# Optimization experiments

Measured on AMD Instinct MI355X. Metric: run time of the kernel, lower is better.

The kernel has to match this reference:

```python
import jax, jax.numpy as jnp
import numpy as np

HIDDEN = 2048
HEAD_DIM = 128
N_HEADS = 16
N_KV_HEADS = 8
Q_DIM = N_HEADS * HEAD_DIM          # 2048
K_DIM = N_KV_HEADS * HEAD_DIM       # 1024
ROPE_THETA = 1.0e6
EPS = 1e-6
T = 4096


def setup_inputs() -> dict:
    key = jax.random.key(0)
    ks = jax.random.split(key, 4)
    x = jax.random.normal(ks[0], (T, HIDDEN), dtype=jnp.float32)
    qkv_w = jax.random.normal(ks[1], (Q_DIM + 2 * K_DIM, HIDDEN), dtype=jnp.float32) * 0.02
    o_w = jax.random.normal(ks[2], (HIDDEN, Q_DIM), dtype=jnp.float32) * 0.02
    q_norm_w = jnp.ones((HEAD_DIM,), dtype=jnp.float32)
    k_norm_w = jnp.ones((HEAD_DIM,), dtype=jnp.float32)
    positions = jnp.arange(T, dtype=jnp.int64 if jax.config.jax_enable_x64 else jnp.int32)
    return {"x": x, "qkv_w": qkv_w, "q_norm_w": q_norm_w,
            "k_norm_w": k_norm_w, "o_w": o_w, "positions": positions}


def _rms_norm(v, w):
    # v: [T, H, D]; normalize over last dim
    var = jnp.mean(v * v, axis=-1, keepdims=True)
    return v * jax.lax.rsqrt(var + EPS) * w


def _rope(v, cos, sin):
    # neox style: rotate halves. v: [T, H, D]; cos/sin: [T, 1, D/2]
    half = v.shape[-1] // 2
    v1, v2 = v[..., :half], v[..., half:]
    return jnp.concatenate([v1 * cos - v2 * sin, v2 * cos + v1 * sin], axis=-1)


def reference(x, qkv_w, q_norm_w, k_norm_w, o_w, positions):
    t = x.shape[0]
    qkv = x @ qkv_w.T                                   # [T, Q_DIM+2*K_DIM]
    q = qkv[:, :Q_DIM].reshape(t, N_HEADS, HEAD_DIM)
    k = qkv[:, Q_DIM:Q_DIM + K_DIM].reshape(t, N_KV_HEADS, HEAD_DIM)
    v = qkv[:, Q_DIM + K_DIM:].reshape(t, N_KV_HEADS, HEAD_DIM)

    q = _rms_norm(q, q_norm_w)
    k = _rms_norm(k, k_norm_w)

    half = HEAD_DIM // 2
    inv_freq = 1.0 / (ROPE_THETA ** (jnp.arange(0, half, dtype=jnp.float32) / half))
    freqs = positions.astype(jnp.float32)[:, None] * inv_freq[None, :]  # [T, half]
    cos = jnp.cos(freqs)[:, None, :]                     # [T, 1, half]
    sin = jnp.sin(freqs)[:, None, :]
    q = _rope(q, cos, sin)
    k = _rope(k, cos, sin)

    # GQA: each kv head serves N_HEADS // N_KV_HEADS query heads
    rep = N_HEADS // N_KV_HEADS
    k = jnp.repeat(k, rep, axis=1)                       # [T, N_HEADS, D]
    v = jnp.repeat(v, rep, axis=1)

    scale = 1.0 / np.sqrt(HEAD_DIM)
    scores = jnp.einsum('thd,shd->hts', q, k) * scale    # [H, T, T]
    causal = positions[:, None] >= positions[None, :]    # [T, T]
    scores = jnp.where(causal[None, :, :], scores, jnp.float32(-1e9))
    attn = jax.nn.softmax(scores, axis=-1)
    o = jnp.einsum('hts,shd->thd', attn, v)              # [T, H, D]
    o = o.reshape(t, Q_DIM)
    return o @ o_w.T                                     # [T, HIDDEN]
```

## Files before the change

### kernel.cpp

```cpp
#include <hip/hip_runtime.h>

#define Tq   4096
#define HIDN 2048
#define NHEAD 16
#define NKV  8
#define DH   128
#define QKVN 4096

typedef unsigned short u16;
typedef unsigned int   u32;
typedef __attribute__((ext_vector_type(8))) __bf16 bf16x8;
typedef __attribute__((ext_vector_type(8))) u16    u16x8;
typedef __attribute__((ext_vector_type(4))) float  f32x4;

#define GLD16(gp, lp) __builtin_amdgcn_global_load_lds( \
    (const __attribute__((address_space(1))) void*)(gp), \
    (__attribute__((address_space(3))) void*)(lp), 16, 0, 0)

__device__ __forceinline__ u16 f2bf(float f) {
  union { float f; u32 u; } v; v.f = f;
  return (u16)((v.u + 0x7fffu + ((v.u >> 16) & 1u)) >> 16);
}
__device__ __forceinline__ float bf2f(u32 bits) {
  union { u32 u; float f; } v; v.u = bits << 16;
  return v.f;
}

__global__ __launch_bounds__(256) void cast_bf16_kernel(const float* __restrict__ in,
                                                        u16* __restrict__ out, int n) {
  int i = (blockIdx.x * 256 + threadIdx.x) * 8;
  if (i >= n) return;
  f32x4 a = *(const f32x4*)(in + i);
  f32x4 b = *(const f32x4*)(in + i + 4);
  u16x8 o;
  #pragma unroll
  for (int j = 0; j < 4; ++j) { o[j] = f2bf(a[j]); o[4 + j] = f2bf(b[j]); }
  *(u16x8*)(out + i) = o;
}

template<bool OUT_BF16>
__global__ __launch_bounds__(256) void gemm_bt_kernel(const u16* __restrict__ A,
                                                      const u16* __restrict__ B,
                                                      void* __restrict__ Cout,
                                                      int M, int N, int K) {
  __shared__ u16 As[128 * 32];
  __shared__ u16 Bs[128 * 32];
  const int tid = threadIdx.x;
  const int lane = tid & 63, wv = tid >> 6;
  const int wr = wv >> 1, wc = wv & 1;
  const int g = lane >> 4, c = lane & 15;
  const int nbn = N >> 7;
  const int bm = blockIdx.x / nbn, bn = blockIdx.x % nbn;
  const int m0 = bm << 7, n0 = bn << 7;

  const int srow = tid >> 2;
  const int sk8 = (tid & 3) * 8;
  const u16* gA0 = A + (size_t)(m0 + srow) * K + sk8;
  const u16* gA1 = gA0 + (size_t)64 * K;
  const u16* gB0 = B + (size_t)(n0 + srow) * K + sk8;
  const u16* gB1 = gB0 + (size_t)64 * K;
  u16* lA0 = As + (wv * 64) * 8;
  u16* lA1 = As + (wv * 64 + 256) * 8;
  u16* lB0 = Bs + (wv * 64) * 8;
  u16* lB1 = Bs + (wv * 64 + 256) * 8;

  f32x4 acc[4][4] = {};

  for (int kt = 0; kt < K; kt += 32) {
    __syncthreads();
    GLD16(gA0 + kt, lA0); GLD16(gA1 + kt, lA1);
    GLD16(gB0 + kt, lB0); GLD16(gB1 + kt, lB1);
    __syncthreads();
    bf16x8 af[4], bfr[4];
    #pragma unroll
    for (int mi = 0; mi < 4; ++mi)
      af[mi] = *(const bf16x8*)&As[(wr * 64 + mi * 16 + c) * 32 + g * 8];
    #pragma unroll
    for (int ni = 0; ni < 4; ++ni)
      bfr[ni] = *(const bf16x8*)&Bs[(wc * 64 + ni * 16 + c) * 32 + g * 8];
    #pragma unroll
    for (int mi = 0; mi < 4; ++mi)
      #pragma unroll
      for (int ni = 0; ni < 4; ++ni)
        acc[mi][ni] = __builtin_amdgcn_mfma_f32_16x16x32_bf16(af[mi], bfr[ni], acc[mi][ni], 0, 0, 0);
  }

  #pragma unroll
  for (int mi = 0; mi < 4; ++mi)
    #pragma unroll
    for (int ni = 0; ni < 4; ++ni) {
      const int row = m0 + wr * 64 + mi * 16 + 4 * g;
      const int col = n0 + wc * 64 + ni * 16 + c;
      #pragma unroll
      for (int j = 0; j < 4; ++j) {
        if (OUT_BF16) ((u16*)Cout)[(size_t)(row + j) * N + col] = f2bf(acc[mi][ni][j]);
        else          ((float*)Cout)[(size_t)(row + j) * N + col] = acc[mi][ni][j];
      }
    }
}

__global__ __launch_bounds__(256) void normrope_kernel(u16* __restrict__ qkv,
                                                       const float* __restrict__ qw,
                                                       const float* __restrict__ kw) {
  const int tid = threadIdx.x, lane = tid & 63, wv = tid >> 6;
  const int wid = blockIdx.x * 4 + wv;
  const int t = wid / 24;
  const int hh = wid % 24;
  const int off = (hh < 16) ? hh * DH : 2048 + (hh - 16) * DH;
  const float* w = (hh < 16) ? qw : kw;
  u16* base = qkv + (size_t)t * QKVN + off;
  const int d0 = lane * 2;

  u32 raw = *(const u32*)(base + d0);
  float v0 = bf2f(raw & 0xffffu), v1 = bf2f(raw >> 16);
  float ss = v0 * v0 + v1 * v1;
  #pragma unroll
  for (int m = 1; m <= 32; m <<= 1) ss += __shfl_xor(ss, m);
  const float rn = rsqrtf(ss * (1.0f / 128.0f) + 1e-6f);
  float n0 = v0 * rn * w[d0];
  float n1 = v1 * rn * w[d0 + 1];
  float o0 = __shfl_xor(n0, 32);
  float o1 = __shfl_xor(n1, 32);
  const int j0 = (lane & 31) * 2;
  const float p = (float)t;
  const float lf = 0.31143075889568947f;
  float a0 = p * __builtin_exp2f(-lf * (float)j0);
  float a1 = p * __builtin_exp2f(-lf * (float)(j0 + 1));
  float c0 = cosf(a0), s0 = sinf(a0), c1 = cosf(a1), s1 = sinf(a1);
  float r0, r1;
  if (lane < 32) { r0 = n0 * c0 - o0 * s0; r1 = n1 * c1 - o1 * s1; }
  else           { r0 = n0 * c0 + o0 * s0; r1 = n1 * c1 + o1 * s1; }
  *(u32*)(base + d0) = (u32)f2bf(r0) | ((u32)f2bf(r1) << 16);
}

__global__ __launch_bounds__(256) void vtrans_kernel(const u16* __restrict__ qkv,
                                                     u16* __restrict__ vt) {
  __shared__ u16 tile[64][72];
  const int tid = threadIdx.x;
  const int b = blockIdx.x;
  const int kvh = b >> 7;
  const int r = b & 127;
  const int t0 = (r & 63) * 64;
  const int d0 = (r >> 6) * 64;
  #pragma unroll
  for (int i = 0; i < 2; ++i) {
    int cidx = tid + i * 256;
    int trow = cidx >> 3, dcol = (cidx & 7) * 8;
    u16x8 v = *(const u16x8*)&qkv[(size_t)(t0 + trow) * QKVN + 3072 + kvh * DH + d0 + dcol];
    *(u16x8*)&tile[trow][dcol] = v;
  }
  __syncthreads();
  #pragma unroll
  for (int i = 0; i < 2; ++i) {
    int cidx = tid + i * 256;
    int drow = cidx >> 3, tcol = (cidx & 7) * 8;
    u16x8 v;
    #pragma unroll
    for (int j = 0; j < 8; ++j) v[j] = tile[tcol + j][drow];
    *(u16x8*)&vt[(size_t)kvh * DH * Tq + (size_t)(d0 + drow) * Tq + t0 + tcol] = v;
  }
}

__global__ __launch_bounds__(256) void attn4_kernel(const u16* __restrict__ qkv,
                                                    const u16* __restrict__ vt,
                                                    u16* __restrict__ o) {
  __shared__ u16 Ks[64 * 128];
  __shared__ u16 Vs[144 * 64];
  __shared__ u16 Ps[4][16][72];
  const int tid = threadIdx.x, lane = tid & 63, wv = tid >> 6;
  const int g = lane >> 4, c = lane & 15;
  const int bid = blockIdx.x;
  const int head = bid & 15;
  const int p = bid >> 4;
  const int kvh = head >> 1;
  const float c2 = 0.08838834764831845f * 1.4426950408889634f;
  const float THR = 40.0f;
  const int xk = c & 7;

  for (int i = tid; i < 16 * 64; i += 256) Vs[128 * 64 + i] = (i < 64) ? 0x3F80 : 0;

  int kOff[4], kDst[4], vOff[4], vDst[4];
  #pragma unroll
  for (int j = 0; j < 4; ++j) {
    int i = j * 256 + tid;
    int kr = i >> 4, kcc = i & 15;
    kOff[j] = kr * QKVN + 2048 + kvh * DH + kcc * 8;
    kDst[j] = kr * 128 + ((kcc ^ (kr & 7)) * 8);
    int vr = i >> 3, vcc = i & 7;
    vOff[j] = vr * Tq + vcc * 8;
    vDst[j] = vr * 64 + ((vcc ^ (vr & 7)) * 8);
  }
  const u16* vkv = vt + (size_t)kvh * DH * Tq;
  u16x8 kreg[4], vreg[4];

  #pragma unroll 1
  for (int seg = 0; seg < 2; ++seg) {
    const int qt = seg ? (63 - p) : p;
    const int q0w = qt * 64 + wv * 16;
    const int nkvb = qt + 1;

    bf16x8 qf[4];
    #pragma unroll
    for (int ks = 0; ks < 4; ++ks)
      qf[ks] = *(const bf16x8*)&qkv[(size_t)(q0w + c) * QKVN + head * DH + ks * 32 + g * 8];

    f32x4 oacc[9] = {};
    float mrow[4] = { -3e38f, -3e38f, -3e38f, -3e38f };

    #pragma unroll
    for (int j = 0; j < 4; ++j) {
      kreg[j] = *(const u16x8*)(qkv + kOff[j]);
      vreg[j] = *(const u16x8*)(vkv + vOff[j]);
    }

    for (int kb = 0; kb < nkvb; ++kb) {
      const int kv0 = kb * 64;
      #pragma unroll
      for (int j = 0; j < 4; ++j) {
        *(u16x8*)&Ks[kDst[j]] = kreg[j];
        *(u16x8*)&Vs[vDst[j]] = vreg[j];
      }
      __syncthreads();
      {
        const int kvn = (kb + 1 < nkvb) ? (kv0 + 64) : kv0;
        #pragma unroll
        for (int j = 0; j < 4; ++j) {
          kreg[j] = *(const u16x8*)(qkv + (size_t)kvn * QKVN + kOff[j]);
          vreg[j] = *(const u16x8*)(vkv + kvn + vOff[j]);
        }
      }
      if (kv0 <= q0w + 15) {
        f32x4 s[4] = {};
        #pragma unroll
        for (int st = 0; st < 4; ++st)
          #pragma unroll
          for (int ks = 0; ks < 4; ++ks) {
            bf16x8 kf = *(const bf16x8*)&Ks[(st * 16 + c) * 128 + (((ks * 4 + g) ^ xk) * 8)];
            s[st] = __builtin_amdgcn_mfma_f32_16x16x32_bf16(qf[ks], kf, s[st], 0, 0, 0);
          }
        if (kv0 + 63 > q0w) {
          #pragma unroll
          for (int st = 0; st < 4; ++st) {
            const int kvc = kv0 + st * 16 + c;
            #pragma unroll
            for (int j = 0; j < 4; ++j)
              if (kvc > q0w + 4 * g + j) s[st][j] = -1e9f;
          }
        }
        float mx[4];
        int need = 0;
        #pragma unroll
        for (int j = 0; j < 4; ++j) {
          float m3 = fmaxf(fmaxf(s[0][j], s[1][j]), fmaxf(s[2][j], s[3][j]));
          m3 = fmaxf(m3, __shfl_xor(m3, 1));
          m3 = fmaxf(m3, __shfl_xor(m3, 2));
          m3 = fmaxf(m3, __shfl_xor(m3, 4));
          m3 = fmaxf(m3, __shfl_xor(m3, 8));
          mx[j] = m3;
          need |= (m3 > mrow[j] + THR);
        }
        if (__any(need)) {
          #pragma unroll
          for (int j = 0; j < 4; ++j) {
            const float mn = fmaxf(mrow[j], mx[j]);
            const float alpha = __builtin_exp2f(c2 * (mrow[j] - mn));
            mrow[j] = mn;
            #pragma unroll
            for (int db = 0; db < 9; ++db) oacc[db][j] *= alpha;
          }
        }
        #pragma unroll
        for (int j = 0; j < 4; ++j) {
          const float cm = c2 * mrow[j];
          #pragma unroll
          for (int st = 0; st < 4; ++st)
            s[st][j] = __builtin_exp2f(c2 * s[st][j] - cm);
        }
        #pragma unroll
        for (int st = 0; st < 4; ++st) {
          u32 pk01, pk23;
          asm("v_cvt_pk_bf16_f32 %0, %1, %2" : "=v"(pk01) : "v"(s[st][0]), "v"(s[st][1]));
          asm("v_cvt_pk_bf16_f32 %0, %1, %2" : "=v"(pk23) : "v"(s[st][2]), "v"(s[st][3]));
          Ps[wv][4 * g + 0][st * 16 + c] = (u16)pk01;
          Ps[wv][4 * g + 1][st * 16 + c] = (u16)(pk01 >> 16);
          Ps[wv][4 * g + 2][st * 16 + c] = (u16)pk23;
          Ps[wv][4 * g + 3][st * 16 + c] = (u16)(pk23 >> 16);
        }
        bf16x8 pa0 = *(const bf16x8*)&Ps[wv][c][g * 8];
        bf16x8 pa1 = *(const bf16x8*)&Ps[wv][c][32 + g * 8];
        #pragma unroll
        for (int db = 0; db < 9; ++db) {
          bf16x8 vf0 = *(const bf16x8*)&Vs[(db * 16 + c) * 64 + ((g ^ xk) * 8)];
          oacc[db] = __builtin_amdgcn_mfma_f32_16x16x32_bf16(pa0, vf0, oacc[db], 0, 0, 0);
          bf16x8 vf1 = *(const bf16x8*)&Vs[(db * 16 + c) * 64 + (((4 + g) ^ xk) * 8)];
          oacc[db] = __builtin_amdgcn_mfma_f32_16x16x32_bf16(pa1, vf1, oacc[db], 0, 0, 0);
        }
      }
      __syncthreads();
    }

    #pragma unroll
    for (int j = 0; j < 4; ++j) {
      const float ls = __shfl(oacc[8][j], lane & 48);
      const float inv = 1.0f / ls;
      #pragma unroll
      for (int db = 0; db < 8; ++db)
        o[(size_t)(q0w + 4 * g + j) * HIDN + head * DH + db * 16 + c] = f2bf(oacc[db][j] * inv);
    }
  }
}

extern "C" void kernel_launch(void* const* d_in, const int* in_sizes, int n_in,
                              void* d_out, int out_size, void* d_ws, size_t ws_size,
                              hipStream_t stream) {
  const float* x    = (const float*)d_in[0];
  const float* qkvw = (const float*)d_in[1];
  const float* qnw  = (const float*)d_in[2];
  const float* knw  = (const float*)d_in[3];
  const float* ow   = (const float*)d_in[4];

  char* ws = (char*)d_ws;
  u16* xb   = (u16*)ws;
  u16* wb   = (u16*)(ws + (16u << 20));
  u16* qkvb = (u16*)(ws + (32u << 20));
  u16* vtb  = (u16*)(ws + (64u << 20));
  u16* owb  = xb;
  u16* ob   = wb;

  cast_bf16_kernel<<<4096, 256, 0, stream>>>(x,    xb, Tq * HIDN);
  cast_bf16_kernel<<<4096, 256, 0, stream>>>(qkvw, wb, QKVN * HIDN);
  gemm_bt_kernel<true><<<1024, 256, 0, stream>>>(xb, wb, (void*)qkvb, Tq, QKVN, HIDN);
  normrope_kernel<<<24576, 256, 0, stream>>>(qkvb, qnw, knw);
  vtrans_kernel<<<1024, 256, 0, stream>>>(qkvb, vtb);
  cast_bf16_kernel<<<2048, 256, 0, stream>>>(ow, owb, HIDN * HIDN);
  attn4_kernel<<<512, 256, 0, stream>>>(qkvb, vtb, ob);
  gemm_bt_kernel<false><<<512, 256, 0, stream>>>(ob, owb, d_out, Tq, HIDN, HIDN);
}
```

Before: 468.3 us.

## Process 128-row query tiles per block with two row groups per wave

The attention kernel now gives each block one 128-row query tile, with each wave owning 32 query rows as two 16-row groups. Before, each block handled two 64-row tiles paired for causal balance. Every K/V fragment loaded from LDS now feeds two MFMAs, halving LDS traffic and the K/V global reload per query row. Blocks are ordered largest-first to help balance the uneven causal work. The cost is doubled accumulator registers (two sets of 9 f32x4), which may lower occupancy, and diagonal blocks do more masked work.

```diff
diff --git a/kernel.cpp b/kernel.cpp
--- a/kernel.cpp
+++ b/kernel.cpp
@@ -161,17 +161,17 @@
   }
 }
 
-__global__ __launch_bounds__(256) void attn4_kernel(const u16* __restrict__ qkv,
+__global__ __launch_bounds__(256) void attn5_kernel(const u16* __restrict__ qkv,
                                                     const u16* __restrict__ vt,
                                                     u16* __restrict__ o) {
   __shared__ u16 Ks[64 * 128];
   __shared__ u16 Vs[144 * 64];
-  __shared__ u16 Ps[4][16][72];
+  __shared__ u16 Ps[4][2][16][72];
   const int tid = threadIdx.x, lane = tid & 63, wv = tid >> 6;
   const int g = lane >> 4, c = lane & 15;
   const int bid = blockIdx.x;
   const int head = bid & 15;
-  const int p = bid >> 4;
+  const int qt = 31 - (bid >> 4);
   const int kvh = head >> 1;
   const float c2 = 0.08838834764831845f * 1.4426950408889634f;
   const float THR = 40.0f;
@@ -193,121 +193,139 @@
   const u16* vkv = vt + (size_t)kvh * DH * Tq;
   u16x8 kreg[4], vreg[4];
 
-  #pragma unroll 1
-  for (int seg = 0; seg < 2; ++seg) {
-    const int qt = seg ? (63 - p) : p;
-    const int q0w = qt * 64 + wv * 16;
-    const int nkvb = qt + 1;
-
-    bf16x8 qf[4];
+  const int q0w = qt * 128 + wv * 32;
+  const int nkvb = qt * 2 + 2;
+
+  bf16x8 qf[2][4];
+  #pragma unroll
+  for (int r = 0; r < 2; ++r)
     #pragma unroll
     for (int ks = 0; ks < 4; ++ks)
-      qf[ks] = *(const bf16x8*)&qkv[(size_t)(q0w + c) * QKVN + head * DH + ks * 32 + g * 8];
-
-    f32x4 oacc[9] = {};
-    float mrow[4] = { -3e38f, -3e38f, -3e38f, -3e38f };
-
+      qf[r][ks] = *(const bf16x8*)&qkv[(size_t)(q0w + r * 16 + c) * QKVN + head * DH + ks * 32 + g * 8];
+
+  f32x4 oacc[2][9] = {};
+  float mrow[2][4] = {{ -3e38f, -3e38f, -3e38f, -3e38f },
+                      { -3e38f, -3e38f, -3e38f, -3e38f }};
+
+  #pragma unroll
+  for (int j = 0; j < 4; ++j) {
+    kreg[j] = *(const u16x8*)(qkv + kOff[j]);
+    vreg[j] = *(const u16x8*)(vkv + vOff[j]);
+  }
+
+  for (int kb = 0; kb < nkvb; ++kb) {
+    const int kv0 = kb * 64;
     #pragma unroll
     for (int j = 0; j < 4; ++j) {
-      kreg[j] = *(const u16x8*)(qkv + kOff[j]);
-      vreg[j] = *(const u16x8*)(vkv + vOff[j]);
-    }
-
-    for (int kb = 0; kb < nkvb; ++kb) {
-      const int kv0 = kb * 64;
+      *(u16x8*)&Ks[kDst[j]] = kreg[j];
+      *(u16x8*)&Vs[vDst[j]] = vreg[j];
+    }
+    __syncthreads();
+    {
+      const int kvn = (kb + 1 < nkvb) ? (kv0 + 64) : kv0;
       #pragma unroll
       for (int j = 0; j < 4; ++j) {
-        *(u16x8*)&Ks[kDst[j]] = kreg[j];
-        *(u16x8*)&Vs[vDst[j]] = vreg[j];
-      }
-      __syncthreads();
-      {
-        const int kvn = (kb + 1 < nkvb) ? (kv0 + 64) : kv0;
-        #pragma unroll
-        for (int j = 0; j < 4; ++j) {
-          kreg[j] = *(const u16x8*)(qkv + (size_t)kvn * QKVN + kOff[j]);
-          vreg[j] = *(const u16x8*)(vkv + kvn + vOff[j]);
+        kreg[j] = *(const u16x8*)(qkv + (size_t)kvn * QKVN + kOff[j]);
+        vreg[j] = *(const u16x8*)(vkv + kvn + vOff[j]);
+      }
+    }
+    if (kv0 <= q0w + 31) {
+      f32x4 s[2][4] = {};
+      #pragma unroll
+      for (int st = 0; st < 4; ++st)
+        #pragma unroll
+        for (int ks = 0; ks < 4; ++ks) {
+          bf16x8 kf = *(const bf16x8*)&Ks[(st * 16 + c) * 128 + (((ks * 4 + g) ^ xk) * 8)];
+          s[0][st] = __builtin_amdgcn_mfma_f32_16x16x32_bf16(qf[0][ks], kf, s[0][st], 0, 0, 0);
+          s[1][st] = __builtin_amdgcn_mfma_f32_16x16x32_bf16(qf[1][ks], kf, s[1][st], 0, 0, 0);
         }
-      }
-      if (kv0 <= q0w + 15) {
-        f32x4 s[4] = {};
-        #pragma unroll
-        for (int st = 0; st < 4; ++st)
-          #pragma unroll
-          for (int ks = 0; ks < 4; ++ks) {
-            bf16x8 kf = *(const bf16x8*)&Ks[(st * 16 + c) * 128 + (((ks * 4 + g) ^ xk) * 8)];
-            s[st] = __builtin_amdgcn_mfma_f32_16x16x32_bf16(qf[ks], kf, s[st], 0, 0, 0);
-          }
-        if (kv0 + 63 > q0w) {
+      if (kv0 + 63 > q0w) {
+        #pragma unroll
+        for (int r = 0; r < 2; ++r)
           #pragma unroll
           for (int st = 0; st < 4; ++st) {
             const int kvc = kv0 + st * 16 + c;
             #pragma unroll
             for (int j = 0; j < 4; ++j)
-              if (kvc > q0w + 4 * g + j) s[st][j] = -1e9f;
+              if (kvc > q0w + r * 16 + 4 * g + j) s[r][st][j] = -1e9f;
           }
-        }
-        float mx[4];
-        int need = 0;
+      }
+      float mx[2][4];
+      int need = 0;
+      #pragma unroll
+      for (int r = 0; r < 2; ++r)
         #pragma unroll
         for (int j = 0; j < 4; ++j) {
-          float m3 = fmaxf(fmaxf(s[0][j], s[1][j]), fmaxf(s[2][j], s[3][j]));
+          float m3 = fmaxf(fmaxf(s[r][0][j], s[r][1][j]), fmaxf(s[r][2][j], s[r][3][j]));
           m3 = fmaxf(m3, __shfl_xor(m3, 1));
           m3 = fmaxf(m3, __shfl_xor(m3, 2));
           m3 = fmaxf(m3, __shfl_xor(m3, 4));
           m3 = fmaxf(m3, __shfl_xor(m3, 8));
-          mx[j] = m3;
-          need |= (m3 > mrow[j] + THR);
+          mx[r][j] = m3;
+          need |= (m3 > mrow[r][j] + THR);
         }
-        if (__any(need)) {
+      if (__any(need)) {
+        #pragma unroll
+        for (int r = 0; r < 2; ++r)
           #pragma unroll
           for (int j = 0; j < 4; ++j) {
-            const float mn = fmaxf(mrow[j], mx[j]);
-            const float alpha = __builtin_exp2f(c2 * (mrow[j] - mn));
-            mrow[j] = mn;
+            const float mn = fmaxf(mrow[r][j], mx[r][j]);
+            const float alpha = __builtin_exp2f(c2 * (mrow[r][j] - mn));
+            mrow[r][j] = mn;
             #pragma unroll
-            for (int db = 0; db < 9; ++db) oacc[db][j] *= alpha;
+            for (int db = 0; db < 9; ++db) oacc[r][db][j] *= alpha;
           }
-        }
+      }
+      #pragma unroll
+      for (int r = 0; r < 2; ++r) {
         #pragma unroll
         for (int j = 0; j < 4; ++j) {
-          const float cm = c2 * mrow[j];
+          const float cm = c2 * mrow[r][j];
           #pragma unroll
           for (int st = 0; st < 4; ++st)
-            s[st][j] = __builtin_exp2f(c2 * s[st][j] - cm);
+            s[r][st][j] = __builtin_exp2f(c2 * s[r][st][j] - cm);
         }
         #pragma unroll
         for (int st = 0; st < 4; ++st) {
           u32 pk01, pk23;
-          asm("v_cvt_pk_bf16_f32 %0, %1, %2" : "=v"(pk01) : "v"(s[st][0]), "v"(s[st][1]));
-          asm("v_cvt_pk_bf16_f32 %0, %1, %2" : "=v"(pk23) : "v"(s[st][2]), "v"(s[st][3]));
-          Ps[wv][4 * g + 0][st * 16 + c] = (u16)pk01;
-          Ps[wv][4 * g + 1][st * 16 + c] = (u16)(pk01 >> 16);
-          Ps[wv][4 * g + 2][st * 16 + c] = (u16)pk23;
-          Ps[wv][4 * g + 3][st * 16 + c] = (u16)(pk23 >> 16);
+          asm("v_cvt_pk_bf16_f32 %0, %1, %2" : "=v"(pk01) : "v"(s[r][st][0]), "v"(s[r][st][1]));
+          asm("v_cvt_pk_bf16_f32 %0, %1, %2" : "=v"(pk23) : "v"(s[r][st][2]), "v"(s[r][st][3]));
+          Ps[wv][r][4 * g + 0][st * 16 + c] = (u16)pk01;
+          Ps[wv][r][4 * g + 1][st * 16 + c] = (u16)(pk01 >> 16);
+          Ps[wv][r][4 * g + 2][st * 16 + c] = (u16)pk23;
+          Ps[wv][r][4 * g + 3][st * 16 + c] = (u16)(pk23 >> 16);
         }
-        bf16x8 pa0 = *(const bf16x8*)&Ps[wv][c][g * 8];
-        bf16x8 pa1 = *(const bf16x8*)&Ps[wv][c][32 + g * 8];
-        #pragma unroll
-        for (int db = 0; db < 9; ++db) {
-          bf16x8 vf0 = *(const bf16x8*)&Vs[(db * 16 + c) * 64 + ((g ^ xk) * 8)];
-          oacc[db] = __builtin_amdgcn_mfma_f32_16x16x32_bf16(pa0, vf0, oacc[db], 0, 0, 0);
-          bf16x8 vf1 = *(const bf16x8*)&Vs[(db * 16 + c) * 64 + (((4 + g) ^ xk) * 8)];
-          oacc[db] = __builtin_amdgcn_mfma_f32_16x16x32_bf16(pa1, vf1, oacc[db], 0, 0, 0);
-        }
-      }
-      __syncthreads();
-    }
-
+      }
+      bf16x8 pa[2][2];
+      #pragma unroll
+      for (int r = 0; r < 2; ++r) {
+        pa[r][0] = *(const bf16x8*)&Ps[wv][r][c][g * 8];
+        pa[r][1] = *(const bf16x8*)&Ps[wv][r][c][32 + g * 8];
+      }
+      #pragma unroll
+      for (int db = 0; db < 9; ++db) {
+        bf16x8 vf0 = *(const bf16x8*)&Vs[(db * 16 + c) * 64 + ((g ^ xk) * 8)];
+        oacc[0][db] = __builtin_amdgcn_mfma_f32_16x16x32_bf16(pa[0][0], vf0, oacc[0][db], 0, 0, 0);
+        oacc[1][db] = __builtin_amdgcn_mfma_f32_16x16x32_bf16(pa[1][0], vf0, oacc[1][db], 0, 0, 0);
+        bf16x8 vf1 = *(const bf16x8*)&Vs[(db * 16 + c) * 64 + (((4 + g) ^ xk) * 8)];
+        oacc[0][db] = __builtin_amdgcn_mfma_f32_16x16x32_bf16(pa[0][1], vf1, oacc[0][db], 0, 0, 0);
+        oacc[1][db] = __builtin_amdgcn_mfma_f32_16x16x32_bf16(pa[1][1], vf1, oacc[1][db], 0, 0, 0);
+      }
+    }
+    __syncthreads();
+  }
+
+  #pragma unroll
+  for (int r = 0; r < 2; ++r)
     #pragma unroll
     for (int j = 0; j < 4; ++j) {
-      const float ls = __shfl(oacc[8][j], lane & 48);
+      const float ls = __shfl(oacc[r][8][j], lane & 48);
       const float inv = 1.0f / ls;
       #pragma unroll
       for (int db = 0; db < 8; ++db)
-        o[(size_t)(q0w + 4 * g + j) * HIDN + head * DH + db * 16 + c] = f2bf(oacc[db][j] * inv);
-    }
-  }
+        o[(size_t)(q0w + r * 16 + 4 * g + j) * HIDN + head * DH + db * 16 + c] =
+            f2bf(oacc[r][db][j] * inv);
+    }
 }
 
 extern "C" void kernel_launch(void* const* d_in, const int* in_sizes, int n_in,
@@ -333,6 +351,6 @@
   normrope_kernel<<<24576, 256, 0, stream>>>(qkvb, qnw, knw);
   vtrans_kernel<<<1024, 256, 0, stream>>>(qkvb, vtb);
   cast_bf16_kernel<<<2048, 256, 0, stream>>>(ow, owb, HIDN * HIDN);
-  attn4_kernel<<<512, 256, 0, stream>>>(qkvb, vtb, ob);
+  attn5_kernel<<<512, 256, 0, stream>>>(qkvb, vtb, ob);
   gemm_bt_kernel<false><<<512, 256, 0, stream>>>(ob, owb, d_out, Tq, HIDN, HIDN);
 }
```

New measurement: 509.9 us. 8.9% more time.
